# Kernel optimization log

Measured on AMD Instinct MI355X. Metric: run time of the kernel, lower is better.

## Reference

```python
import jax, jax.numpy as jnp
import numpy as np

B, L, D_MODEL = 4, 4096, 128
D_INNER, D_STATE, DT_RANK, D_CONV = 256, 16, 8, 4
EPS = 1e-5


def setup_inputs() -> dict:
    key = jax.random.key(0)
    ks = jax.random.split(key, 10)
    s = lambda *sh: 0.02
    inp = {
        'x': jax.random.normal(ks[0], (B, L, D_MODEL), jnp.float32),
        'norm_w': jnp.ones((D_MODEL,), jnp.float32),
        # Linear weights stored as (in, out) so y = x @ W
        'in_proj_w': jax.random.normal(ks[1], (D_MODEL, 2 * D_INNER), jnp.float32) * 0.02,
        'conv_w': jax.random.normal(ks[2], (D_INNER, D_CONV), jnp.float32) * 0.2,
        'conv_b': jnp.zeros((D_INNER,), jnp.float32),
        'x_proj_w': jax.random.normal(ks[3], (D_INNER, DT_RANK + 2 * D_STATE), jnp.float32) * 0.02,
        'dt_proj_w': jax.random.normal(ks[4], (DT_RANK, D_INNER), jnp.float32) * 0.1,
        'dt_proj_b': jnp.zeros((D_INNER,), jnp.float32),
        'A_log': jnp.log(jnp.tile(jnp.arange(1, D_STATE + 1, dtype=jnp.float32)[None, :], (D_INNER, 1))),
        'D': jnp.ones((D_INNER,), jnp.float32),
        'out_proj_w': jax.random.normal(ks[5], (D_INNER, D_MODEL), jnp.float32) * 0.02,
    }
    return inp


def _mamba_block(x, norm_w, in_proj_w, conv_w, conv_b, x_proj_w,
                 dt_proj_w, dt_proj_b, A_log, D, out_proj_w):
    b, l, d = x.shape
    # RMSNorm
    h = x * jax.lax.rsqrt(jnp.mean(x * x, axis=-1, keepdims=True) + EPS) * norm_w
    # in_proj -> split into x path and residual gate
    xr = h @ in_proj_w                      # (b, l, 2*d_inner)
    xi, res = jnp.split(xr, 2, axis=-1)
    # depthwise causal conv1d over time
    xc = jnp.transpose(xi, (0, 2, 1))       # (b, d_inner, l)
    kernel = conv_w[:, None, :]             # (d_inner, 1, d_conv)
    xc = jax.lax.conv_general_dilated(
        xc, kernel, window_strides=(1,), padding=[(D_CONV - 1, 0)],
        feature_group_count=D_INNER,
        dimension_numbers=('NCH', 'OIH', 'NCH')) + conv_b[None, :, None]
    xc = jnp.transpose(xc, (0, 2, 1))       # (b, l, d_inner)
    xc = jax.nn.silu(xc)
    # SSM parameterization
    A = -jnp.exp(A_log.astype(jnp.float32))           # (d_inner, n)
    x_dbl = xc @ x_proj_w                              # (b, l, dt_rank + 2n)
    delta = x_dbl[..., :DT_RANK]
    Bmat = x_dbl[..., DT_RANK:DT_RANK + D_STATE]       # (b, l, n)
    Cmat = x_dbl[..., DT_RANK + D_STATE:]              # (b, l, n)
    delta = jax.nn.softplus(delta @ dt_proj_w + dt_proj_b)  # (b, l, d_inner)
    # discretize
    deltaA = jnp.exp(jnp.einsum('bld,dn->bldn', delta, A))  # (b, l, d_inner, n)
    deltaB_u = delta[..., None] * Bmat[:, :, None, :] * xc[..., None]
    # selective scan over time (lax.scan replaces the Python loop)
    def step(s, inputs):
        dA_t, dBu_t, C_t = inputs
        s = dA_t * s + dBu_t                     # (b, d_inner, n)
        y_t = jnp.einsum('bdn,bn->bd', s, C_t)   # (b, d_inner)
        return s, y_t
    s0 = jnp.zeros((b, D_INNER, D_STATE), xc.dtype)
    scan_in = (jnp.transpose(deltaA, (1, 0, 2, 3)),
               jnp.transpose(deltaB_u, (1, 0, 2, 3)),
               jnp.transpose(Cmat, (1, 0, 2)))
    _, ys = jax.lax.scan(step, s0, scan_in)      # (l, b, d_inner)
    y = jnp.transpose(ys, (1, 0, 2)) + xc * D    # (b, l, d_inner)
    y = y * jax.nn.silu(res)
    return y @ out_proj_w + x                    # residual add


def reference(x, norm_w, in_proj_w, conv_w, conv_b, x_proj_w,
              dt_proj_w, dt_proj_b, A_log, D, out_proj_w):
    return _mamba_block(x, norm_w, in_proj_w, conv_w, conv_b, x_proj_w,
                        dt_proj_w, dt_proj_b, A_log, D, out_proj_w)
```

## Files before the change

kernel.cpp:

```cpp
#include <hip/hip_runtime.h>
#include <math.h>

#define B_    4
#define L_    4096
#define DM    128
#define DI    256
#define DS    16
#define DTR   8
#define XPN   (DTR + 2*DS)
#define NB    (DI + 2*DS)
#define M_    (B_*L_)
#define CHUNK 32
#define NC    (L_/CHUNK)
#define LOG2E 1.4426950408889634f
#define PREP_N (512*128 + NB*DI + DM*DI)

typedef __attribute__((ext_vector_type(8))) short bf16x8;
typedef __attribute__((ext_vector_type(4))) float f32x4;
typedef unsigned short ushort_t;

__device__ __forceinline__ ushort_t f2bf(float f) {
  unsigned int u = __float_as_uint(f);
  u += 0x7FFFu + ((u >> 16) & 1u);
  return (ushort_t)(u >> 16);
}
__device__ __forceinline__ float bf2f(ushort_t u) {
  return __uint_as_float(((unsigned int)u) << 16);
}

__global__ __launch_bounds__(256) void prep_rms_kernel(const float* __restrict__ x,
                                                       const float* __restrict__ nw,
                                                       const float* __restrict__ inW,
                                                       const float* __restrict__ Wx,
                                                       const float* __restrict__ Wdt,
                                                       const float* __restrict__ outw,
                                                       ushort_t* __restrict__ xbf,
                                                       ushort_t* __restrict__ inWt,
                                                       ushort_t* __restrict__ WbigT,
                                                       ushort_t* __restrict__ outWt) {
  if (blockIdx.x < M_ / 4) {
    int row  = blockIdx.x * 4 + (threadIdx.x >> 6);
    int lane = threadIdx.x & 63;
    const float* xp = x + (size_t)row * DM;
    float v0 = xp[lane], v1 = xp[lane + 64];
    float s = v0 * v0 + v1 * v1;
    #pragma unroll
    for (int off = 32; off > 0; off >>= 1) s += __shfl_xor(s, off);
    float r = rsqrtf(s / DM + 1e-5f);
    ushort_t* op = xbf + (size_t)row * DM;
    op[lane]      = f2bf(v0 * r * nw[lane]);
    op[lane + 64] = f2bf(v1 * r * nw[lane + 64]);
    return;
  }
  int g = (blockIdx.x - M_ / 4) * 256 + threadIdx.x;
  if (g < 512 * 128) {
    int n = g >> 7, k = g & 127;
    inWt[g] = f2bf(inW[k * 512 + n]);
  } else if (g < 512 * 128 + NB * DI) {
    int q = g - 512 * 128;
    int c = q >> 8, k = q & 255;
    float v;
    if (c < DI) {
      v = 0.f;
      #pragma unroll
      for (int j = 0; j < DTR; ++j) v = fmaf(Wx[k * XPN + j], Wdt[j * DI + c], v);
    } else {
      v = Wx[k * XPN + DTR + (c - DI)];
    }
    WbigT[q] = f2bf(v);
  } else if (g < PREP_N) {
    int q = g - (512 * 128 + NB * DI);
    int n = q >> 8, k = q & 255;
    outWt[q] = f2bf(outw[k * DM + n]);
  }
}

__global__ __launch_bounds__(256) void g1_conv_kernel(const ushort_t* __restrict__ A,
                                                      const ushort_t* __restrict__ Wt,
                                                      const float* __restrict__ cw,
                                                      const float* __restrict__ cb,
                                                      ushort_t* __restrict__ xcbf,
                                                      ushort_t* __restrict__ resbf) {
  constexpr int KK = 128, NT = 4;
  __shared__ __align__(16) char smem_raw[35648];
  ushort_t (*Asm)[145][8] = (ushort_t (*)[145][8])smem_raw;
  ushort_t (*Bx)[65][8]   = (ushort_t (*)[65][8])(smem_raw + 18560);
  ushort_t (*Br)[65][8]   = (ushort_t (*)[65][8])(smem_raw + 26880);
  float* T = (float*)smem_raw;
  const int tid  = threadIdx.x;
  const int wave = tid >> 6, lane = tid & 63;
  const int quad = lane >> 4, l16 = lane & 15;
  const int row0 = blockIdx.x * 128;
  const int by   = blockIdx.y;
  const int c0x  = by * 64;
  const int c0r  = 256 + by * 64;
  const bool zpad = (row0 & (L_ - 1)) == 0;
  f32x4 ax[2][NT], ar[2][NT], acc2[NT];
  #pragma unroll
  for (int mt = 0; mt < 2; ++mt)
    #pragma unroll
    for (int nt = 0; nt < NT; ++nt) {
      ax[mt][nt] = (f32x4){0.f, 0.f, 0.f, 0.f};
      ar[mt][nt] = (f32x4){0.f, 0.f, 0.f, 0.f};
    }
  #pragma unroll
  for (int nt = 0; nt < NT; ++nt) acc2[nt] = (f32x4){0.f, 0.f, 0.f, 0.f};

  for (int k0 = 0; k0 < KK; k0 += 64) {
    #pragma unroll
    for (int i = 0; i < 5; ++i) {
      int q = tid + i * 256;
      if (i < 4 || tid < 128) {
        int m = q >> 3, kb = q & 7;
        bf16x8 v = {0, 0, 0, 0, 0, 0, 0, 0};
        if (!(zpad && m < 16))
          v = *(const bf16x8*)(A + (size_t)(row0 - 16 + m) * KK + k0 + kb * 8);
        *(bf16x8*)(&Asm[kb][m][0]) = v;
      }
    }
    #pragma unroll
    for (int i = 0; i < 2; ++i) {
      int q = tid + i * 256;
      int n = q >> 3, kb = q & 7;
      *(bf16x8*)(&Bx[kb][n][0]) =
          *(const bf16x8*)(Wt + (size_t)(c0x + n) * KK + k0 + kb * 8);
    }
    #pragma unroll
    for (int i = 0; i < 2; ++i) {
      int q = tid + i * 256;
      int n = q >> 3, kb = q & 7;
      *(bf16x8*)(&Br[kb][n][0]) =
          *(const bf16x8*)(Wt + (size_t)(c0r + n) * KK + k0 + kb * 8);
    }
    __syncthreads();
    #pragma unroll
    for (int ks = 0; ks < 2; ++ks) {
      bf16x8 af[2], bx[NT], br[NT];
      #pragma unroll
      for (int mt = 0; mt < 2; ++mt)
        af[mt] = *(const bf16x8*)(&Asm[ks * 4 + quad][16 + wave * 32 + mt * 16 + l16][0]);
      #pragma unroll
      for (int nt = 0; nt < NT; ++nt) {
        bx[nt] = *(const bf16x8*)(&Bx[ks * 4 + quad][nt * 16 + l16][0]);
        br[nt] = *(const bf16x8*)(&Br[ks * 4 + quad][nt * 16 + l16][0]);
      }
      #pragma unroll
      for (int mt = 0; mt < 2; ++mt)
        #pragma unroll
        for (int nt = 0; nt < NT; ++nt) {
          ax[mt][nt] = __builtin_amdgcn_mfma_f32_16x16x32_bf16(af[mt], bx[nt],
                                                               ax[mt][nt], 0, 0, 0);
          ar[mt][nt] = __builtin_amdgcn_mfma_f32_16x16x32_bf16(af[mt], br[nt],
                                                               ar[mt][nt], 0, 0, 0);
        }
      if (wave == 0) {
        bf16x8 ab = *(const bf16x8*)(&Asm[ks * 4 + quad][l16][0]);
        #pragma unroll
        for (int nt = 0; nt < NT; ++nt)
          acc2[nt] = __builtin_amdgcn_mfma_f32_16x16x32_bf16(ab, bx[nt],
                                                             acc2[nt], 0, 0, 0);
      }
    }
    __syncthreads();
  }

  #pragma unroll
  for (int mt = 0; mt < 2; ++mt)
    #pragma unroll
    for (int nt = 0; nt < NT; ++nt) {
      int col   = c0x + nt * 16 + l16;
      int rbase = row0 + wave * 32 + mt * 16 + quad * 4;
      #pragma unroll
      for (int r = 0; r < 4; ++r)
        resbf[(size_t)(rbase + r) * DI + col] = f2bf(ar[mt][nt][r]);
    }

  #pragma unroll
  for (int mt = 0; mt < 2; ++mt)
    #pragma unroll
    for (int nt = 0; nt < NT; ++nt)
      #pragma unroll
      for (int r = 0; r < 4; ++r)
        T[(3 + wave * 32 + mt * 16 + quad * 4 + r) * 68 + nt * 16 + l16] =
            ax[mt][nt][r];
  if (wave == 0 && quad == 3) {
    #pragma unroll
    for (int nt = 0; nt < NT; ++nt)
      #pragma unroll
      for (int r = 1; r < 4; ++r)
        T[(r - 1) * 68 + nt * 16 + l16] = acc2[nt][r];
  }
  __syncthreads();
  {
    const int c   = tid & 63;
    const int R0  = (tid >> 6) * 32;
    const int dch = c0x + c;
    float4 w4   = *(const float4*)(cw + dch * 4);
    float bias  = cb[dch];
    float t0 = T[(R0 + 0) * 68 + c];
    float t1 = T[(R0 + 1) * 68 + c];
    float t2 = T[(R0 + 2) * 68 + c];
    for (int rr = 0; rr < 32; ++rr) {
      float t3 = T[(R0 + rr + 3) * 68 + c];
      float s = fmaf(w4.x, t0, fmaf(w4.y, t1, fmaf(w4.z, t2, fmaf(w4.w, t3, bias))));
      float v = s / (1.f + __expf(-s));
      xcbf[(size_t)(row0 + R0 + rr) * DI + dch] = f2bf(v);
      t0 = t1; t1 = t2; t2 = t3;
    }
  }
}

__global__ __launch_bounds__(512, 4) void scanA_kernel(
    const ushort_t* __restrict__ xcbf, const ushort_t* __restrict__ WbigT,
    const float* __restrict__ bdt, const float* __restrict__ Alog,
    ushort_t* __restrict__ deltab, ushort_t* __restrict__ Bmb,
    ushort_t* __restrict__ Cmb, float2* __restrict__ PS) {
  __shared__ __align__(16) ushort_t Asm[32][33][8];
  __shared__ float T[32][257];
  __shared__ float Bs[32][20], Cs[32][20];
  const int tid  = threadIdx.x;
  const int wave = tid >> 6, lane = tid & 63;
  const int quad = lane >> 4, l16 = lane & 15;
  const int b = blockIdx.x >> 7, c = blockIdx.x & (NC - 1);
  const size_t rowbase = (size_t)b * L_ + (size_t)c * CHUNK;
  const int d  = (wave << 5) | (lane & 31);
  const int nh = lane >> 5;
  const int n0 = nh * 8;

  {
    int m = tid & 31, kb = tid >> 5;
    *(bf16x8*)(&Asm[kb][m][0]) =
        *(const bf16x8*)(xcbf + (rowbase + m) * DI + kb * 8);
    *(bf16x8*)(&Asm[kb + 16][m][0]) =
        *(const bf16x8*)(xcbf + (rowbase + m) * DI + (kb + 16) * 8);
  }
  __syncthreads();

  for (int tp = wave; tp < 36; tp += 8) {
    int mt = tp / 18, nt = tp % 18;
    f32x4 acc = {0.f, 0.f, 0.f, 0.f};
    #pragma unroll
    for (int ks = 0; ks < 8; ++ks) {
      bf16x8 af = *(const bf16x8*)(&Asm[ks * 4 + quad][mt * 16 + l16][0]);
      bf16x8 bf = *(const bf16x8*)(WbigT + (size_t)(nt * 16 + l16) * DI + ks * 32 + quad * 8);
      acc = __builtin_amdgcn_mfma_f32_16x16x32_bf16(af, bf, acc, 0, 0, 0);
    }
    int row = mt * 16 + quad * 4;
    if (nt < 16) {
      int col = nt * 16 + l16;
      float bb = bdt[col];
      #pragma unroll
      for (int r = 0; r < 4; ++r) {
        float v = acc[r] + bb;
        T[row + r][col] = (v > 20.f) ? v : log1pf(__expf(v));
      }
    } else if (nt == 16) {
      #pragma unroll
      for (int r = 0; r < 4; ++r) Bs[row + r][l16] = acc[r];
    } else {
      #pragma unroll
      for (int r = 0; r < 4; ++r) Cs[row + r][l16] = acc[r];
    }
  }
  __syncthreads();

  #pragma unroll
  for (int i = 0; i < 8; ++i) {
    int idx2 = tid + i * 512;
    int row = idx2 >> 7, cp = idx2 & 127;
    unsigned int pk = (unsigned int)f2bf(T[row][2 * cp]) |
                      ((unsigned int)f2bf(T[row][2 * cp + 1]) << 16);
    *(unsigned int*)(deltab + (rowbase + row) * DI + 2 * cp) = pk;
  }
  {
    int row = tid >> 4, n = tid & 15;
    Bmb[rowbase * DS + tid] = f2bf(Bs[row][n]);
    Cmb[rowbase * DS + tid] = f2bf(Cs[row][n]);
  }

  float c0 = -__expf(Alog[d * DS]) * LOG2E;
  float aln[8];
  #pragma unroll
  for (int j = 0; j < 8; ++j) aln[j] = -__expf(Alog[d * DS + n0 + j]) * LOG2E;
  bool geom = true;
  #pragma unroll
  for (int j = 0; j < 8; ++j)
    geom = geom && (fabsf(aln[j] - (n0 + j + 1) * c0) <= 1e-3f * fabsf(aln[j]));

  float P[8], S[8];
  #pragma unroll
  for (int j = 0; j < 8; ++j) { P[j] = 1.f; S[j] = 0.f; }
  #pragma unroll 4
  for (int t = 0; t < CHUNK; ++t) {
    float dl = T[t][d];
    float xv = bf2f(Asm[d >> 3][t][d & 7]);
    float du = dl * xv;
    float Bv[8];
    *(float4*)&Bv[0] = *(const float4*)&Bs[t][n0];
    *(float4*)&Bv[4] = *(const float4*)&Bs[t][n0 + 4];
    if (geom) {
      float e1 = exp2f(dl * c0);
      float a;
      if (nh) { float e2 = e1 * e1, e4 = e2 * e2; a = e4 * e4 * e1; }
      else a = e1;
      #pragma unroll
      for (int j = 0; j < 8; ++j) {
        P[j] *= a;
        S[j] = fmaf(a, S[j], du * Bv[j]);
        a *= e1;
      }
    } else {
      #pragma unroll
      for (int j = 0; j < 8; ++j) {
        float a = exp2f(dl * aln[j]);
        P[j] *= a;
        S[j] = fmaf(a, S[j], du * Bv[j]);
      }
    }
  }
  size_t ob = ((size_t)(b * NC + c) << 12) + ((nh * 256 + d) << 3);
  float4* p4 = (float4*)(PS + ob);
  p4[0] = make_float4(P[0], S[0], P[1], S[1]);
  p4[1] = make_float4(P[2], S[2], P[3], S[3]);
  p4[2] = make_float4(P[4], S[4], P[5], S[5]);
  p4[3] = make_float4(P[6], S[6], P[7], S[7]);
}

__global__ __launch_bounds__(1024) void scanB_kernel(const float2* __restrict__ PS,
                                                     float* __restrict__ sinit) {
  __shared__ float Ps[16][64], Ss[16][64];
  const int tid = threadIdx.x;
  const int seg = tid >> 6;
  const int j   = tid & 63;
  const int b   = blockIdx.x >> 6;
  const int dn  = ((blockIdx.x & 63) << 6) + j;
  const size_t base = ((size_t)(b * NC + seg * 8) << 12) + (size_t)dn;
  float Pk[8], Sk[8];
  #pragma unroll
  for (int k = 0; k < 8; ++k) {
    float2 v = PS[base + ((size_t)k << 12)];
    Pk[k] = v.x; Sk[k] = v.y;
  }
  float Pg = 1.f, Sg = 0.f;
  #pragma unroll
  for (int k = 0; k < 8; ++k) { Sg = fmaf(Pk[k], Sg, Sk[k]); Pg *= Pk[k]; }
  Ps[seg][j] = Pg; Ss[seg][j] = Sg;
  __syncthreads();
  #pragma unroll
  for (int off = 1; off < 16; off <<= 1) {
    float Pp = 1.f, Sp = 0.f;
    if (seg >= off) { Pp = Ps[seg - off][j]; Sp = Ss[seg - off][j]; }
    __syncthreads();
    if (seg >= off) {
      Sg = fmaf(Pg, Sp, Sg); Pg *= Pp;
      Ps[seg][j] = Pg; Ss[seg][j] = Sg;
    }
    __syncthreads();
  }
  float s = (seg == 0) ? 0.f : Ss[seg - 1][j];
  #pragma unroll
  for (int k = 0; k < 8; ++k) {
    sinit[base + ((size_t)k << 12)] = s;
    s = fmaf(Pk[k], s, Sk[k]);
  }
}

__global__ __launch_bounds__(512, 4) void scanC_kernel(
    const ushort_t* __restrict__ deltab, const ushort_t* __restrict__ xcbf,
    const ushort_t* __restrict__ Bmb, const ushort_t* __restrict__ Cmb,
    const float* __restrict__ Alog, const float* __restrict__ Dp,
    const ushort_t* __restrict__ resbf, const float* __restrict__ sinit,
    const ushort_t* __restrict__ outWt, const float* __restrict__ x,
    float* __restrict__ out) {
  __shared__ float Bs[32][20], Cs[32][20];
  __shared__ __align__(16) ushort_t Dl[32][264];
  __shared__ __align__(16) ushort_t Xc[32][264];
  const int tid  = threadIdx.x;
  const int wave = tid >> 6, lane = tid & 63;
  const int quad = lane >> 4, l16 = lane & 15;
  const int b = blockIdx.x >> 7, c = blockIdx.x & (NC - 1);
  const size_t rowbase = (size_t)b * L_ + (size_t)c * CHUNK;
  const int d  = (wave << 5) | (lane & 31);
  const int nh = lane >> 5;
  const int n0 = nh * 8;
  {
    int row = tid >> 4, n = tid & 15;
    Bs[row][n] = bf2f(Bmb[rowbase * DS + tid]);
    Cs[row][n] = bf2f(Cmb[rowbase * DS + tid]);
  }
  {
    int kb = tid & 31, m = tid >> 5;
    *(bf16x8*)(&Dl[m][kb * 8]) =
        *(const bf16x8*)(deltab + (rowbase + m) * DI + kb * 8);
    *(bf16x8*)(&Dl[m + 16][kb * 8]) =
        *(const bf16x8*)(deltab + (rowbase + m + 16) * DI + kb * 8);
    *(bf16x8*)(&Xc[m][kb * 8]) =
        *(const bf16x8*)(xcbf + (rowbase + m) * DI + kb * 8);
    *(bf16x8*)(&Xc[m + 16][kb * 8]) =
        *(const bf16x8*)(xcbf + (rowbase + m + 16) * DI + kb * 8);
  }
  float c0 = -__expf(Alog[d * DS]) * LOG2E;
  float aln[8];
  #pragma unroll
  for (int j = 0; j < 8; ++j) aln[j] = -__expf(Alog[d * DS + n0 + j]) * LOG2E;
  bool geom = true;
  #pragma unroll
  for (int j = 0; j < 8; ++j)
    geom = geom && (fabsf(aln[j] - (n0 + j + 1) * c0) <= 1e-3f * fabsf(aln[j]));
  const float Dd = Dp[d];
  float S[8];
  {
    size_t ib = ((size_t)(b * NC + c) << 12) + ((nh * 256 + d) << 3);
    float4 v0 = *(const float4*)(sinit + ib);
    float4 v1 = *(const float4*)(sinit + ib + 4);
    S[0] = v0.x; S[1] = v0.y; S[2] = v0.z; S[3] = v0.w;
    S[4] = v1.x; S[5] = v1.y; S[6] = v1.z; S[7] = v1.w;
  }
  __syncthreads();
  #pragma unroll 4
  for (int t = 0; t < CHUNK; ++t) {
    float dl = bf2f(Dl[t][d]);
    float xv = bf2f(Xc[t][d]);
    float du = dl * xv;
    float Bv[8], Cv[8];
    *(float4*)&Bv[0] = *(const float4*)&Bs[t][n0];
    *(float4*)&Bv[4] = *(const float4*)&Bs[t][n0 + 4];
    *(float4*)&Cv[0] = *(const float4*)&Cs[t][n0];
    *(float4*)&Cv[4] = *(const float4*)&Cs[t][n0 + 4];
    float y = 0.f;
    if (geom) {
      float e1 = exp2f(dl * c0);
      float a;
      if (nh) { float e2 = e1 * e1, e4 = e2 * e2; a = e4 * e4 * e1; }
      else a = e1;
      #pragma unroll
      for (int j = 0; j < 8; ++j) {
        S[j] = fmaf(a, S[j], du * Bv[j]);
        y = fmaf(S[j], Cv[j], y);
        a *= e1;
      }
    } else {
      #pragma unroll
      for (int j = 0; j < 8; ++j) {
        float a = exp2f(dl * aln[j]);
        S[j] = fmaf(a, S[j], du * Bv[j]);
        y = fmaf(S[j], Cv[j], y);
      }
    }
    float yo = __shfl_xor(y, 32);
    if (nh == 0) {
      float rv = bf2f(resbf[(rowbase + t) * DI + d]);
      float yt = y + yo + xv * Dd;
      float sil = rv / (1.f + __expf(-rv));
      Dl[t][d] = f2bf(yt * sil);
    }
  }
  __syncthreads();
  #pragma unroll
  for (int mt = 0; mt < 2; ++mt) {
    f32x4 acc = {0.f, 0.f, 0.f, 0.f};
    #pragma unroll
    for (int ks = 0; ks < 8; ++ks) {
      bf16x8 af = *(const bf16x8*)(&Dl[mt * 16 + l16][ks * 32 + quad * 8]);
      bf16x8 bf = *(const bf16x8*)(outWt + (size_t)(wave * 16 + l16) * DI + ks * 32 + quad * 8);
      acc = __builtin_amdgcn_mfma_f32_16x16x32_bf16(af, bf, acc, 0, 0, 0);
    }
    int col = wave * 16 + l16;
    size_t rb = rowbase + mt * 16 + quad * 4;
    #pragma unroll
    for (int r = 0; r < 4; ++r)
      out[(rb + r) * DM + col] = acc[r] + x[(rb + r) * DM + col];
  }
}

extern "C" void kernel_launch(void* const* d_in, const int* in_sizes, int n_in,
                              void* d_out, int out_size, void* d_ws, size_t ws_size,
                              hipStream_t stream) {
  const float* x      = (const float*)d_in[0];
  const float* norm_w = (const float*)d_in[1];
  const float* inW    = (const float*)d_in[2];
  const float* convw  = (const float*)d_in[3];
  const float* convb  = (const float*)d_in[4];
  const float* xprojw = (const float*)d_in[5];
  const float* dtw    = (const float*)d_in[6];
  const float* dtb    = (const float*)d_in[7];
  const float* alog   = (const float*)d_in[8];
  const float* Dp     = (const float*)d_in[9];
  const float* outw   = (const float*)d_in[10];
  float* out = (float*)d_out;

  const size_t CS = (size_t)B_ * NC * DI * DS;
  float2* PS    = (float2*)d_ws;
  float* sinit  = (float*)(PS + CS);
  ushort_t* bfbase = (ushort_t*)(sinit + CS);
  ushort_t* xbf    = bfbase;
  ushort_t* xcbf   = xbf + (size_t)M_ * DM;
  ushort_t* resbf  = xcbf + (size_t)M_ * DI;
  ushort_t* deltab = resbf + (size_t)M_ * DI;
  ushort_t* Bmb    = deltab + (size_t)M_ * DI;
  ushort_t* Cmb    = Bmb + (size_t)M_ * DS;
  ushort_t* inWt   = Cmb + (size_t)M_ * DS;
  ushort_t* WbigT  = inWt + 512 * 128;
  ushort_t* outWt  = WbigT + NB * DI;

  prep_rms_kernel<<<M_ / 4 + (PREP_N + 255) / 256, 256, 0, stream>>>(
      x, norm_w, inW, xprojw, dtw, outw, xbf, inWt, WbigT, outWt);
  g1_conv_kernel<<<dim3(M_ / 128, 4), 256, 0, stream>>>(
      xbf, inWt, convw, convb, xcbf, resbf);
  scanA_kernel<<<B_ * NC, 512, 0, stream>>>(
      xcbf, WbigT, dtb, alog, deltab, Bmb, Cmb, PS);
  scanB_kernel<<<B_ * 64, 1024, 0, stream>>>(PS, sinit);
  scanC_kernel<<<B_ * NC, 512, 0, stream>>>(
      deltab, xcbf, Bmb, Cmb, alog, Dp, resbf, sinit, outWt, x, out);
}
```

Before: 161.1 us.

## Double scan threads per block, splitting state dimension into four groups of four

```diff
diff --git a/kernel.cpp b/kernel.cpp
--- a/kernel.cpp
+++ b/kernel.cpp
@@ -210,7 +210,7 @@
   }
 }
 
-__global__ __launch_bounds__(512, 4) void scanA_kernel(
+__global__ __launch_bounds__(1024, 8) void scanA_kernel(
     const ushort_t* __restrict__ xcbf, const ushort_t* __restrict__ WbigT,
     const float* __restrict__ bdt, const float* __restrict__ Alog,
     ushort_t* __restrict__ deltab, ushort_t* __restrict__ Bmb,
@@ -223,20 +223,18 @@
   const int quad = lane >> 4, l16 = lane & 15;
   const int b = blockIdx.x >> 7, c = blockIdx.x & (NC - 1);
   const size_t rowbase = (size_t)b * L_ + (size_t)c * CHUNK;
-  const int d  = (wave << 5) | (lane & 31);
-  const int nh = lane >> 5;
-  const int n0 = nh * 8;
+  const int d  = (wave << 4) | l16;
+  const int g  = quad;
+  const int n0 = g * 4;
 
   {
-    int m = tid & 31, kb = tid >> 5;
+    int m = tid >> 5, kb = tid & 31;
     *(bf16x8*)(&Asm[kb][m][0]) =
         *(const bf16x8*)(xcbf + (rowbase + m) * DI + kb * 8);
-    *(bf16x8*)(&Asm[kb + 16][m][0]) =
-        *(const bf16x8*)(xcbf + (rowbase + m) * DI + (kb + 16) * 8);
-  }
-  __syncthreads();
-
-  for (int tp = wave; tp < 36; tp += 8) {
+  }
+  __syncthreads();
+
+  for (int tp = wave; tp < 36; tp += 16) {
     int mt = tp / 18, nt = tp % 18;
     f32x4 acc = {0.f, 0.f, 0.f, 0.f};
     #pragma unroll
@@ -252,7 +250,7 @@
       #pragma unroll
       for (int r = 0; r < 4; ++r) {
         float v = acc[r] + bb;
-        T[row + r][col] = (v > 20.f) ? v : log1pf(__expf(v));
+        T[row + r][col] = (v > 20.f) ? v : __logf(1.f + __expf(v));
       }
     } else if (nt == 16) {
       #pragma unroll
@@ -265,65 +263,60 @@
   __syncthreads();
 
   #pragma unroll
-  for (int i = 0; i < 8; ++i) {
-    int idx2 = tid + i * 512;
+  for (int i = 0; i < 4; ++i) {
+    int idx2 = tid + i * 1024;
     int row = idx2 >> 7, cp = idx2 & 127;
     unsigned int pk = (unsigned int)f2bf(T[row][2 * cp]) |
                       ((unsigned int)f2bf(T[row][2 * cp + 1]) << 16);
     *(unsigned int*)(deltab + (rowbase + row) * DI + 2 * cp) = pk;
   }
-  {
+  if (tid < CHUNK * DS) {
     int row = tid >> 4, n = tid & 15;
     Bmb[rowbase * DS + tid] = f2bf(Bs[row][n]);
     Cmb[rowbase * DS + tid] = f2bf(Cs[row][n]);
   }
 
   float c0 = -__expf(Alog[d * DS]) * LOG2E;
-  float aln[8];
-  #pragma unroll
-  for (int j = 0; j < 8; ++j) aln[j] = -__expf(Alog[d * DS + n0 + j]) * LOG2E;
+  float aln[4];
+  #pragma unroll
+  for (int j = 0; j < 4; ++j) aln[j] = -__expf(Alog[d * DS + n0 + j]) * LOG2E;
   bool geom = true;
   #pragma unroll
-  for (int j = 0; j < 8; ++j)
+  for (int j = 0; j < 4; ++j)
     geom = geom && (fabsf(aln[j] - (n0 + j + 1) * c0) <= 1e-3f * fabsf(aln[j]));
 
-  float P[8], S[8];
-  #pragma unroll
-  for (int j = 0; j < 8; ++j) { P[j] = 1.f; S[j] = 0.f; }
+  float P[4], S[4];
+  #pragma unroll
+  for (int j = 0; j < 4; ++j) { P[j] = 1.f; S[j] = 0.f; }
   #pragma unroll 4
   for (int t = 0; t < CHUNK; ++t) {
     float dl = T[t][d];
     float xv = bf2f(Asm[d >> 3][t][d & 7]);
     float du = dl * xv;
-    float Bv[8];
+    float Bv[4];
     *(float4*)&Bv[0] = *(const float4*)&Bs[t][n0];
-    *(float4*)&Bv[4] = *(const float4*)&Bs[t][n0 + 4];
     if (geom) {
       float e1 = exp2f(dl * c0);
-      float a;
-      if (nh) { float e2 = e1 * e1, e4 = e2 * e2; a = e4 * e4 * e1; }
-      else a = e1;
-      #pragma unroll
-      for (int j = 0; j < 8; ++j) {
+      float a  = exp2f(dl * aln[0]);
+      #pragma unroll
+      for (int j = 0; j < 4; ++j) {
         P[j] *= a;
         S[j] = fmaf(a, S[j], du * Bv[j]);
         a *= e1;
       }
     } else {
       #pragma unroll
-      for (int j = 0; j < 8; ++j) {
+      for (int j = 0; j < 4; ++j) {
         float a = exp2f(dl * aln[j]);
         P[j] *= a;
         S[j] = fmaf(a, S[j], du * Bv[j]);
       }
     }
   }
-  size_t ob = ((size_t)(b * NC + c) << 12) + ((nh * 256 + d) << 3);
+  size_t ob = ((size_t)(b * NC + c) << 12) + ((g * 256 + d) << 2);
   float4* p4 = (float4*)(PS + ob);
   p4[0] = make_float4(P[0], S[0], P[1], S[1]);
   p4[1] = make_float4(P[2], S[2], P[3], S[3]);
-  p4[2] = make_float4(P[4], S[4], P[5], S[5]);
-  p4[3] = make_float4(P[6], S[6], P[7], S[7]);
 }
 
 __global__ __launch_bounds__(1024) void scanB_kernel(const float2* __restrict__ PS,
@@ -365,7 +358,7 @@
   }
 }
 
-__global__ __launch_bounds__(512, 4) void scanC_kernel(
+__global__ __launch_bounds__(1024, 8) void scanC_kernel(
     const ushort_t* __restrict__ deltab, const ushort_t* __restrict__ xcbf,
     const ushort_t* __restrict__ Bmb, const ushort_t* __restrict__ Cmb,
     const float* __restrict__ Alog, const float* __restrict__ Dp,
@@ -380,41 +373,35 @@
   const int quad = lane >> 4, l16 = lane & 15;
   const int b = blockIdx.x >> 7, c = blockIdx.x & (NC - 1);
   const size_t rowbase = (size_t)b * L_ + (size_t)c * CHUNK;
-  const int d  = (wave << 5) | (lane & 31);
-  const int nh = lane >> 5;
-  const int n0 = nh * 8;
-  {
+  const int d  = (wave << 4) | l16;
+  const int g  = quad;
+  const int n0 = g * 4;
+  if (tid < CHUNK * DS) {
     int row = tid >> 4, n = tid & 15;
     Bs[row][n] = bf2f(Bmb[rowbase * DS + tid]);
     Cs[row][n] = bf2f(Cmb[rowbase * DS + tid]);
   }
   {
-    int kb = tid & 31, m = tid >> 5;
+    int m = tid >> 5, kb = tid & 31;
     *(bf16x8*)(&Dl[m][kb * 8]) =
         *(const bf16x8*)(deltab + (rowbase + m) * DI + kb * 8);
-    *(bf16x8*)(&Dl[m + 16][kb * 8]) =
-        *(const bf16x8*)(deltab + (rowbase + m + 16) * DI + kb * 8);
     *(bf16x8*)(&Xc[m][kb * 8]) =
         *(const bf16x8*)(xcbf + (rowbase + m) * DI + kb * 8);
-    *(bf16x8*)(&Xc[m + 16][kb * 8]) =
-        *(const bf16x8*)(xcbf + (rowbase + m + 16) * DI + kb * 8);
   }
   float c0 = -__expf(Alog[d * DS]) * LOG2E;
-  float aln[8];
-  #pragma unroll
-  for (int j = 0; j < 8; ++j) aln[j] = -__expf(Alog[d * DS + n0 + j]) * LOG2E;
+  float aln[4];
+  #pragma unroll
+  for (int j = 0; j < 4; ++j) aln[j] = -__expf(Alog[d * DS + n0 + j]) * LOG2E;
   bool geom = true;
   #pragma unroll
-  for (int j = 0; j < 8; ++j)
+  for (int j = 0; j < 4; ++j)
     geom = geom && (fabsf(aln[j] - (n0 + j + 1) * c0) <= 1e-3f * fabsf(aln[j]));
   const float Dd = Dp[d];
-  float S[8];
+  float S[4];
   {
-    size_t ib = ((size_t)(b * NC + c) << 12) + ((nh * 256 + d) << 3);
+    size_t ib = ((size_t)(b * NC + c) << 12) + ((g * 256 + d) << 2);
     float4 v0 = *(const float4*)(sinit + ib);
-    float4 v1 = *(const float4*)(sinit + ib + 4);
     S[0] = v0.x; S[1] = v0.y; S[2] = v0.z; S[3] = v0.w;
-    S[4] = v1.x; S[5] = v1.y; S[6] = v1.z; S[7] = v1.w;
   }
   __syncthreads();
   #pragma unroll 4
@@ -422,50 +409,47 @@
     float dl = bf2f(Dl[t][d]);
     float xv = bf2f(Xc[t][d]);
     float du = dl * xv;
-    float Bv[8], Cv[8];
+    float Bv[4], Cv[4];
     *(float4*)&Bv[0] = *(const float4*)&Bs[t][n0];
-    *(float4*)&Bv[4] = *(const float4*)&Bs[t][n0 + 4];
     *(float4*)&Cv[0] = *(const float4*)&Cs[t][n0];
-    *(float4*)&Cv[4] = *(const float4*)&Cs[t][n0 + 4];
     float y = 0.f;
     if (geom) {
       float e1 = exp2f(dl * c0);
-      float a;
-      if (nh) { float e2 = e1 * e1, e4 = e2 * e2; a = e4 * e4 * e1; }
-      else a = e1;
-      #pragma unroll
-      for (int j = 0; j < 8; ++j) {
+      float a  = exp2f(dl * aln[0]);
+      #pragma unroll
+      for (int j = 0; j < 4; ++j) {
         S[j] = fmaf(a, S[j], du * Bv[j]);
         y = fmaf(S[j], Cv[j], y);
         a *= e1;
       }
     } else {
       #pragma unroll
-      for (int j = 0; j < 8; ++j) {
+      for (int j = 0; j < 4; ++j) {
         float a = exp2f(dl * aln[j]);
         S[j] = fmaf(a, S[j], du * Bv[j]);
         y = fmaf(S[j], Cv[j], y);
       }
     }
-    float yo = __shfl_xor(y, 32);
-    if (nh == 0) {
+    y += __shfl_xor(y, 16);
+    y += __shfl_xor(y, 32);
+    if (g == 0) {
       float rv = bf2f(resbf[(rowbase + t) * DI + d]);
-      float yt = y + yo + xv * Dd;
+      float yt = y + xv * Dd;
       float sil = rv / (1.f + __expf(-rv));
       Dl[t][d] = f2bf(yt * sil);
     }
   }
   __syncthreads();
-  #pragma unroll
-  for (int mt = 0; mt < 2; ++mt) {
+  {
+    int mt = wave >> 3, ct = wave & 7;
     f32x4 acc = {0.f, 0.f, 0.f, 0.f};
     #pragma unroll
     for (int ks = 0; ks < 8; ++ks) {
       bf16x8 af = *(const bf16x8*)(&Dl[mt * 16 + l16][ks * 32 + quad * 8]);
-      bf16x8 bf = *(const bf16x8*)(outWt + (size_t)(wave * 16 + l16) * DI + ks * 32 + quad * 8);
+      bf16x8 bf = *(const bf16x8*)(outWt + (size_t)(ct * 16 + l16) * DI + ks * 32 + quad * 8);
       acc = __builtin_amdgcn_mfma_f32_16x16x32_bf16(af, bf, acc, 0, 0, 0);
     }
-    int col = wave * 16 + l16;
+    int col = ct * 16 + l16;
     size_t rb = rowbase + mt * 16 + quad * 4;
     #pragma unroll
     for (int r = 0; r < 4; ++r)
@@ -507,9 +491,9 @@
       x, norm_w, inW, xprojw, dtw, outw, xbf, inWt, WbigT, outWt);
   g1_conv_kernel<<<dim3(M_ / 128, 4), 256, 0, stream>>>(
       xbf, inWt, convw, convb, xcbf, resbf);
-  scanA_kernel<<<B_ * NC, 512, 0, stream>>>(
+  scanA_kernel<<<B_ * NC, 1024, 0, stream>>>(
       xcbf, WbigT, dtb, alog, deltab, Bmb, Cmb, PS);
   scanB_kernel<<<B_ * 64, 1024, 0, stream>>>(PS, sinit);
-  scanC_kernel<<<B_ * NC, 512, 0, stream>>>(
+  scanC_kernel<<<B_ * NC, 1024, 0, stream>>>(
       deltab, xcbf, Bmb, Cmb, alog, Dp, resbf, sinit, outWt, x, out);
 }
```

After: 170.8 us. 1.06x slower.
